# Performance work log

Measured on AMD Instinct MI355X. Metric: run time of the kernel, lower is better.

## Reference

```python
import jax, jax.numpy as jnp
import numpy as np

WIN = 8
NUM_HEADS = 4
DIM = 128


def _relative_position_index(ws):
    coords = np.stack(np.meshgrid(np.arange(ws), np.arange(ws), indexing='ij'))  # (2, ws, ws)
    cf = coords.reshape(2, -1)                      # (2, ws*ws)
    rel = (cf[:, :, None] - cf[:, None, :]).transpose(1, 2, 0).astype(np.int64)  # (N, N, 2)
    rel[..., 0] += ws - 1
    rel[..., 1] += ws - 1
    rel[..., 0] *= 2 * ws - 1
    return rel.sum(-1)                              # (N, N) int64


def setup_inputs() -> dict:
    key = jax.random.key(0)
    ks = jax.random.split(key, 8)
    B_, N, C = 4096, WIN * WIN, DIM
    nW = 4096
    x = jax.random.normal(ks[0], (B_, N, C), dtype=jnp.float32)
    mask = jax.random.normal(ks[1], (nW, N, N), dtype=jnp.float32)
    wq = jax.random.normal(ks[2], (C, C), dtype=jnp.float32) * 0.02
    bq = jnp.zeros((C,), dtype=jnp.float32)
    wkv = jax.random.normal(ks[3], (2 * C, C), dtype=jnp.float32) * 0.02
    bkv = jnp.zeros((2 * C,), dtype=jnp.float32)
    bias_table = jax.random.normal(ks[4], ((2 * WIN - 1) * (2 * WIN - 1), NUM_HEADS), dtype=jnp.float32) * 0.02
    wproj = jax.random.normal(ks[5], (C, C), dtype=jnp.float32) * 0.02
    bproj = jnp.zeros((C,), dtype=jnp.float32)
    rel_index = jnp.asarray(_relative_position_index(WIN))
    return {"x": x, "wq": wq, "bq": bq, "wkv": wkv, "bkv": bkv,
            "bias_table": bias_table, "wproj": wproj, "bproj": bproj,
            "mask": mask, "rel_index": rel_index}


def reference(x, wq, bq, wkv, bkv, bias_table, wproj, bproj, mask, rel_index):
    B_, N, C = x.shape
    H = NUM_HEADS
    d = C // H
    scale = d ** -0.5
    # qkv projection (attn_kv=None path)
    q = (x @ wq.T + bq).reshape(B_, N, H, d).transpose(0, 2, 1, 3)      # (B_, H, N, d)
    kv = (x @ wkv.T + bkv).reshape(B_, N, 2, H, d)
    k = kv[:, :, 0].transpose(0, 2, 1, 3)                               # (B_, H, N, d)
    v = kv[:, :, 1].transpose(0, 2, 1, 3)
    attn = jnp.einsum('bhnd,bhmd->bhnm', q * scale, k)                  # (B_, H, N, N)
    # relative position bias gather: (N*N,) -> (N, N, H) -> (H, N, N)
    rpb = bias_table[rel_index.reshape(-1)].reshape(N, N, H).transpose(2, 0, 1)
    attn = attn + rpb[None]
    # shifted-window mask: attn viewed as (B_//nW, nW, H, N, N) + mask (nW, 1, N, N)
    nW = mask.shape[0]
    attn = (attn.reshape(B_ // nW, nW, H, N, N) + mask[None, :, None]).reshape(B_, H, N, N)
    attn = jax.nn.softmax(attn, axis=-1)
    out = jnp.einsum('bhnm,bhmd->bhnd', attn, v).transpose(0, 2, 1, 3).reshape(B_, N, C)
    return out @ wproj.T + bproj
```

## Files before the change

### kernel.cpp

```cpp
#include <hip/hip_runtime.h>


typedef __bf16 bf16x8 __attribute__((ext_vector_type(8)));
typedef __bf16 bf16x4 __attribute__((ext_vector_type(4)));
typedef float f32x4 __attribute__((ext_vector_type(4)));

#define LOG2E 1.4426950408889634f
#define QSCALE (0.17677669529663687f * 1.4426950408889634f)

__global__ __launch_bounds__(256)
void prep_kernel(const float* __restrict__ wq,
                 const float* __restrict__ wkv,
                 const float* __restrict__ wp,
                 const float* __restrict__ bt,
                 const int* __restrict__ ri,
                 char* __restrict__ ws) {
  int t = blockIdx.x * 256 + (int)threadIdx.x;
  if (t < 8192) {
    int s = t >> 11;
    int c = t & 2047;
    int lane = c & 63, kk = (c >> 6) & 3, ct = c >> 8;
    int li = lane & 15, q4 = lane >> 4;
    int col = ct * 16 + li;
    int ko = kk * 32 + q4 * 8;
    const float* src = (s == 0) ? (wq + col * 128 + ko)
                     : (s == 1) ? (wkv + col * 128 + ko)
                     : (s == 2) ? (wkv + (col + 128) * 128 + ko)
                                : (wp + col * 128 + ko);
    bf16x8 v;
#pragma unroll
    for (int i = 0; i < 8; ++i) v[i] = (__bf16)src[i];
    *(bf16x8*)(ws + s * 32768 + c * 16) = v;
  } else {
    int c = t - 8192;
    int lane = c & 63, tj = (c >> 6) & 3, ti = (c >> 8) & 3, h = (c >> 10) & 3;
    int li = lane & 15, q4 = lane >> 4;
    int qt = tj * 16 + li;
    f32x4 r;
#pragma unroll
    for (int rr = 0; rr < 4; ++rr) {
      int kt = ti * 16 + q4 * 4 + rr;
      r[rr] = LOG2E * bt[ri[qt * 64 + kt] * 4 + h];
    }
    *(f32x4*)(ws + 131072 + c * 16) = r;
  }
}

static __device__ __forceinline__ bf16x8 cvt8nt(const float* __restrict__ p) {
  f32x4 a = __builtin_nontemporal_load((const f32x4*)p);
  f32x4 b = __builtin_nontemporal_load((const f32x4*)p + 1);
  bf16x8 r;
#pragma unroll
  for (int i = 0; i < 4; ++i) { r[i] = (__bf16)a[i]; r[i + 4] = (__bf16)b[i]; }
  return r;
}

static __device__ __forceinline__ int xaddr(int r, int c) {
  return (r << 8) + ((((c >> 3) ^ (r & 7)) << 4)) + ((c & 7) << 1);
}
static __device__ __forceinline__ int qaddr(int r, int c) {
  return (r << 6) + ((((c >> 3) ^ ((r >> 2) & 3)) << 4)) + ((c & 7) << 1);
}
static __device__ __forceinline__ int paddr(int r, int c) {
  return (r << 7) + ((((c >> 3) ^ (r & 7)) << 4)) + ((c & 7) << 1);
}
static __device__ __forceinline__ int vtaddr(int dd, int m) {
  return (dd << 7) + ((((m >> 3) ^ (dd & 7)) << 4)) + ((m & 7) << 1);
}

#define MFMA16(acc, afr, bfr) \
  acc = __builtin_amdgcn_mfma_f32_16x16x32_bf16(afr, bfr, acc, 0, 0, 0)

__global__ __launch_bounds__(256, 3)
void winattn_kernel(const float* __restrict__ xg,
                    const float* __restrict__ bq,
                    const float* __restrict__ bkv,
                    const float* __restrict__ bp,
                    const float* __restrict__ mask,
                    const char* __restrict__ ws,
                    float* __restrict__ out) {
  __shared__ char smem[49152];
  const int b = blockIdx.x;
  const int tid = (int)threadIdx.x;
  const int h = tid >> 6;
  const int lane = tid & 63;
  const int q4 = lane >> 4;
  const int li = lane & 15;
  const int Wb = 16384 + h * 8192;
  const int Qb = Wb, Kb = Wb + 4096, Pb = Wb;
  const int Vb = h * 4096;
  const bf16x8* __restrict__ wqP = (const bf16x8*)(ws);
  const bf16x8* __restrict__ wkP = (const bf16x8*)(ws + 32768);
  const bf16x8* __restrict__ wvP = (const bf16x8*)(ws + 65536);
  const bf16x8* __restrict__ wpP = (const bf16x8*)(ws + 98304);
  const f32x4* __restrict__ rpbP = (const f32x4*)(ws + 131072);

  {
    const float* xw = xg + b * 8192;
#pragma unroll
    for (int rep = 0; rep < 4; ++rep) {
      int chunk = rep * 256 + tid;
      int r = chunk >> 4, cc = chunk & 15;
      bf16x8 v = cvt8nt(xw + r * 128 + cc * 8);
      *(bf16x8*)(smem + xaddr(r, cc * 8)) = v;
    }
  }
  __syncthreads();

  {
    f32x4 aqT[2][4] = {}; f32x4 akT[2][4] = {}; f32x4 av[4][2] = {};
#pragma unroll
    for (int kk = 0; kk < 4; ++kk) {
      bf16x8 a[4];
#pragma unroll
      for (int nt = 0; nt < 4; ++nt)
        a[nt] = *(const bf16x8*)(smem + xaddr(nt * 16 + li, kk * 32 + q4 * 8));
#pragma unroll
      for (int mt = 0; mt < 2; ++mt) {
        int wi = ((h * 2 + mt) * 4 + kk) * 64 + lane;
        bf16x8 wbq = wqP[wi];
        bf16x8 wbk = wkP[wi];
        bf16x8 wbv = wvP[wi];
#pragma unroll
        for (int nt = 0; nt < 4; ++nt) {
          MFMA16(aqT[mt][nt], wbq, a[nt]);
          MFMA16(akT[mt][nt], wbk, a[nt]);
          MFMA16(av[nt][mt], a[nt], wbv);
        }
      }
    }
#pragma unroll
    for (int mt = 0; mt < 2; ++mt) {
      f32x4 bq4 = *(const f32x4*)(bq + h * 32 + mt * 16 + q4 * 4);
      f32x4 bk4 = *(const f32x4*)(bkv + h * 32 + mt * 16 + q4 * 4);
      int f0 = mt * 16 + q4 * 4;
#pragma unroll
      for (int nt = 0; nt < 4; ++nt) {
        bf16x4 qv, kv;
#pragma unroll
        for (int rr = 0; rr < 4; ++rr) {
          qv[rr] = (__bf16)((aqT[mt][nt][rr] + bq4[rr]) * QSCALE);
          kv[rr] = (__bf16)(akT[mt][nt][rr] + bk4[rr]);
        }
        int row = nt * 16 + li;
        *(bf16x4*)(smem + Qb + qaddr(row, f0)) = qv;
        *(bf16x4*)(smem + Kb + qaddr(row, f0)) = kv;
      }
    }
    __syncthreads();
#pragma unroll
    for (int tj = 0; tj < 2; ++tj) {
      int col = h * 32 + tj * 16 + li;
      float bvv = bkv[col + 128];
      int lc = tj * 16 + li;
#pragma unroll
      for (int ti = 0; ti < 4; ++ti) {
        bf16x4 vv;
#pragma unroll
        for (int rr = 0; rr < 4; ++rr) vv[rr] = (__bf16)(av[ti][tj][rr] + bvv);
        *(bf16x4*)(smem + Vb + vtaddr(lc, ti * 16 + q4 * 4)) = vv;
      }
    }
  }
  asm volatile("s_waitcnt lgkmcnt(0)" ::: "memory");

  f32x4 bias[4][4];
  {
    const float* mw = mask + b * 4096;
#pragma unroll
    for (int ti = 0; ti < 4; ++ti)
#pragma unroll
      for (int tj = 0; tj < 4; ++tj) {
        f32x4 rv = rpbP[((h * 4 + ti) * 4 + tj) * 64 + lane];
        f32x4 mv = __builtin_nontemporal_load(
            (const f32x4*)(mw + (tj * 16 + li) * 64 + ti * 16 + q4 * 4));
#pragma unroll
        for (int rr = 0; rr < 4; ++rr) rv[rr] = fmaf(LOG2E, mv[rr], rv[rr]);
        bias[ti][tj] = rv;
      }
  }

  f32x4 S[4][4];
  {
    bf16x8 qf[4], kf[4];
#pragma unroll
    for (int t = 0; t < 4; ++t) {
      qf[t] = *(const bf16x8*)(smem + Qb + qaddr(t * 16 + li, q4 * 8));
      kf[t] = *(const bf16x8*)(smem + Kb + qaddr(t * 16 + li, q4 * 8));
    }
#pragma unroll
    for (int ti = 0; ti < 4; ++ti)
#pragma unroll
      for (int tj = 0; tj < 4; ++tj)
        S[ti][tj] = __builtin_amdgcn_mfma_f32_16x16x32_bf16(
            kf[ti], qf[tj], bias[ti][tj], 0, 0, 0);
  }

#pragma unroll
  for (int tj = 0; tj < 4; ++tj) {
    float mx = S[0][tj][0];
#pragma unroll
    for (int ti = 0; ti < 4; ++ti)
#pragma unroll
      for (int rr = 0; rr < 4; ++rr) mx = fmaxf(mx, S[ti][tj][rr]);
    mx = fmaxf(mx, __shfl_xor(mx, 16));
    mx = fmaxf(mx, __shfl_xor(mx, 32));
    float s = 0.f;
#pragma unroll
    for (int ti = 0; ti < 4; ++ti)
#pragma unroll
      for (int rr = 0; rr < 4; ++rr) {
        float e = __builtin_amdgcn_exp2f(S[ti][tj][rr] - mx);
        S[ti][tj][rr] = e;
        s += e;
      }
    s += __shfl_xor(s, 16);
    s += __shfl_xor(s, 32);
    float rinv = __builtin_amdgcn_rcpf(s);
#pragma unroll
    for (int ti = 0; ti < 4; ++ti)
#pragma unroll
      for (int rr = 0; rr < 4; ++rr) S[ti][tj][rr] *= rinv;
  }

#pragma unroll
  for (int ti = 0; ti < 4; ++ti)
#pragma unroll
    for (int tj = 0; tj < 4; ++tj) {
      bf16x4 pv;
#pragma unroll
      for (int rr = 0; rr < 4; ++rr) pv[rr] = (__bf16)S[ti][tj][rr];
      *(bf16x4*)(smem + Pb + paddr(tj * 16 + li, ti * 16 + q4 * 4)) = pv;
    }
  asm volatile("s_waitcnt lgkmcnt(0)" ::: "memory");

  f32x4 O[4][2] = {};
#pragma unroll
  for (int ks = 0; ks < 2; ++ks) {
    bf16x8 pf[4], vf[2];
#pragma unroll
    for (int ti = 0; ti < 4; ++ti)
      pf[ti] = *(const bf16x8*)(smem + Pb + paddr(ti * 16 + li, ks * 32 + q4 * 8));
#pragma unroll
    for (int tj = 0; tj < 2; ++tj)
      vf[tj] = *(const bf16x8*)(smem + Vb + vtaddr(tj * 16 + li, ks * 32 + q4 * 8));
#pragma unroll
    for (int ti = 0; ti < 4; ++ti)
#pragma unroll
      for (int tj = 0; tj < 2; ++tj)
        MFMA16(O[ti][tj], pf[ti], vf[tj]);
  }

  __syncthreads();
#pragma unroll
  for (int ti = 0; ti < 4; ++ti)
#pragma unroll
    for (int tj = 0; tj < 2; ++tj)
#pragma unroll
      for (int rr = 0; rr < 4; ++rr) {
        int row = ti * 16 + q4 * 4 + rr;
        int col = h * 32 + tj * 16 + li;
        *(__bf16*)(smem + xaddr(row, col)) = (__bf16)O[ti][tj][rr];
      }
  __syncthreads();

  {
    f32x4 acc[2][4] = {};
#pragma unroll
    for (int kk = 0; kk < 4; ++kk) {
      bf16x8 a[4];
#pragma unroll
      for (int nt = 0; nt < 4; ++nt)
        a[nt] = *(const bf16x8*)(smem + xaddr(nt * 16 + li, kk * 32 + q4 * 8));
#pragma unroll
      for (int mt = 0; mt < 2; ++mt) {
        int wi = ((h * 2 + mt) * 4 + kk) * 64 + lane;
        bf16x8 wb = wpP[wi];
#pragma unroll
        for (int nt = 0; nt < 4; ++nt)
          MFMA16(acc[mt][nt], wb, a[nt]);
      }
    }
    float* ow = out + b * 8192;
#pragma unroll
    for (int mt = 0; mt < 2; ++mt) {
      f32x4 bp4 = *(const f32x4*)(bp + h * 32 + mt * 16 + q4 * 4);
#pragma unroll
      for (int nt = 0; nt < 4; ++nt) {
        f32x4 o;
#pragma unroll
        for (int rr = 0; rr < 4; ++rr) o[rr] = acc[mt][nt][rr] + bp4[rr];
        __builtin_nontemporal_store(
            o, (f32x4*)(ow + (nt * 16 + li) * 128 + h * 32 + mt * 16 + q4 * 4));
      }
    }
  }
}

extern "C" void kernel_launch(void* const* d_in, const int* in_sizes, int n_in,
                              void* d_out, int out_size, void* d_ws, size_t ws_size,
                              hipStream_t stream) {
  (void)in_sizes; (void)n_in; (void)ws_size; (void)out_size;
  prep_kernel<<<96, 256, 0, stream>>>(
      (const float*)d_in[1],
      (const float*)d_in[3],
      (const float*)d_in[6],
      (const float*)d_in[5],
      (const int*)d_in[9],
      (char*)d_ws);
  winattn_kernel<<<4096, 256, 0, stream>>>(
      (const float*)d_in[0],
      (const float*)d_in[2],
      (const float*)d_in[4],
      (const float*)d_in[7],
      (const float*)d_in[8],
      (const char*)d_ws,
      (float*)d_out);
}
```

Baseline: 389.3 us.

## Process four windows per block with register-prefetched next-window input

Each block now loops over four windows instead of one. While the current window is computed, the next window's x tile is loaded into registers and written to a separate shared-memory region once the QKV stage is done, so global load latency overlaps compute. Shared memory grows to 64KB, occupancy drops to 2 blocks per CU, and the grid shrinks to 1024 blocks. Nontemporal loads and stores are replaced by ordinary ones. Fewer resident waves and extra register pressure from the prefetch buffer may limit latency hiding.

```diff
diff --git a/kernel.cpp b/kernel.cpp
--- a/kernel.cpp
+++ b/kernel.cpp
@@ -46,15 +46,6 @@
   }
 }
 
-static __device__ __forceinline__ bf16x8 cvt8nt(const float* __restrict__ p) {
-  f32x4 a = __builtin_nontemporal_load((const f32x4*)p);
-  f32x4 b = __builtin_nontemporal_load((const f32x4*)p + 1);
-  bf16x8 r;
-#pragma unroll
-  for (int i = 0; i < 4; ++i) { r[i] = (__bf16)a[i]; r[i + 4] = (__bf16)b[i]; }
-  return r;
-}
-
 static __device__ __forceinline__ int xaddr(int r, int c) {
   return (r << 8) + ((((c >> 3) ^ (r & 7)) << 4)) + ((c & 7) << 1);
 }
@@ -71,7 +62,7 @@
 #define MFMA16(acc, afr, bfr) \
   acc = __builtin_amdgcn_mfma_f32_16x16x32_bf16(afr, bfr, acc, 0, 0, 0)
 
-__global__ __launch_bounds__(256, 3)
+__global__ __launch_bounds__(256, 2)
 void winattn_kernel(const float* __restrict__ xg,
                     const float* __restrict__ bq,
                     const float* __restrict__ bkv,
@@ -79,79 +70,126 @@
                     const float* __restrict__ mask,
                     const char* __restrict__ ws,
                     float* __restrict__ out) {
-  __shared__ char smem[49152];
-  const int b = blockIdx.x;
+  __shared__ char smem[65536];
   const int tid = (int)threadIdx.x;
   const int h = tid >> 6;
   const int lane = tid & 63;
   const int q4 = lane >> 4;
   const int li = lane & 15;
-  const int Wb = 16384 + h * 8192;
-  const int Qb = Wb, Kb = Wb + 4096, Pb = Wb;
-  const int Vb = h * 4096;
+  const int YB = 16384;
+  const int Vb = 16384 + h * 4096;
+  const int Qb = 32768 + h * 8192;
+  const int Kb = Qb + 4096;
+  const int Pb = Qb;
   const bf16x8* __restrict__ wqP = (const bf16x8*)(ws);
   const bf16x8* __restrict__ wkP = (const bf16x8*)(ws + 32768);
   const bf16x8* __restrict__ wvP = (const bf16x8*)(ws + 65536);
   const bf16x8* __restrict__ wpP = (const bf16x8*)(ws + 98304);
   const f32x4* __restrict__ rpbP = (const f32x4*)(ws + 131072);
 
+  const int b0 = blockIdx.x * 4;
+  f32x4 px[8];
+
   {
-    const float* xw = xg + b * 8192;
+    const float* xw = xg + (size_t)b0 * 8192;
 #pragma unroll
     for (int rep = 0; rep < 4; ++rep) {
-      int chunk = rep * 256 + tid;
-      int r = chunk >> 4, cc = chunk & 15;
-      bf16x8 v = cvt8nt(xw + r * 128 + cc * 8);
+      int ch = rep * 256 + tid;
+      int r = ch >> 4, cc = ch & 15;
+      px[2 * rep] = *(const f32x4*)(xw + r * 128 + cc * 8);
+      px[2 * rep + 1] = *(const f32x4*)(xw + r * 128 + cc * 8 + 4);
+    }
+#pragma unroll
+    for (int rep = 0; rep < 4; ++rep) {
+      int ch = rep * 256 + tid;
+      int r = ch >> 4, cc = ch & 15;
+      bf16x8 v;
+#pragma unroll
+      for (int i = 0; i < 4; ++i) {
+        v[i] = (__bf16)px[2 * rep][i];
+        v[i + 4] = (__bf16)px[2 * rep + 1][i];
+      }
       *(bf16x8*)(smem + xaddr(r, cc * 8)) = v;
     }
   }
   __syncthreads();
 
-  {
-    f32x4 aqT[2][4] = {}; f32x4 akT[2][4] = {}; f32x4 av[4][2] = {};
-#pragma unroll
-    for (int kk = 0; kk < 4; ++kk) {
-      bf16x8 a[4];
-#pragma unroll
-      for (int nt = 0; nt < 4; ++nt)
-        a[nt] = *(const bf16x8*)(smem + xaddr(nt * 16 + li, kk * 32 + q4 * 8));
+#pragma unroll 1
+  for (int it = 0; it < 4; ++it) {
+    const int b = b0 + it;
+
+    if (it < 3) {
+      const float* xw = xg + (size_t)(b + 1) * 8192;
+#pragma unroll
+      for (int rep = 0; rep < 4; ++rep) {
+        int ch = rep * 256 + tid;
+        int r = ch >> 4, cc = ch & 15;
+        px[2 * rep] = *(const f32x4*)(xw + r * 128 + cc * 8);
+        px[2 * rep + 1] = *(const f32x4*)(xw + r * 128 + cc * 8 + 4);
+      }
+    }
+
+    f32x4 av[4][2] = {};
+    {
+      f32x4 aqT[2][4] = {}; f32x4 akT[2][4] = {};
+#pragma unroll
+      for (int kk = 0; kk < 4; ++kk) {
+        bf16x8 a[4];
+#pragma unroll
+        for (int nt = 0; nt < 4; ++nt)
+          a[nt] = *(const bf16x8*)(smem + xaddr(nt * 16 + li, kk * 32 + q4 * 8));
+#pragma unroll
+        for (int mt = 0; mt < 2; ++mt) {
+          int wi = ((h * 2 + mt) * 4 + kk) * 64 + lane;
+          bf16x8 wbq = wqP[wi];
+          bf16x8 wbk = wkP[wi];
+          bf16x8 wbv = wvP[wi];
+#pragma unroll
+          for (int nt = 0; nt < 4; ++nt) {
+            MFMA16(aqT[mt][nt], wbq, a[nt]);
+            MFMA16(akT[mt][nt], wbk, a[nt]);
+            MFMA16(av[nt][mt], a[nt], wbv);
+          }
+        }
+      }
 #pragma unroll
       for (int mt = 0; mt < 2; ++mt) {
-        int wi = ((h * 2 + mt) * 4 + kk) * 64 + lane;
-        bf16x8 wbq = wqP[wi];
-        bf16x8 wbk = wkP[wi];
-        bf16x8 wbv = wvP[wi];
+        f32x4 bq4 = *(const f32x4*)(bq + h * 32 + mt * 16 + q4 * 4);
+        f32x4 bk4 = *(const f32x4*)(bkv + h * 32 + mt * 16 + q4 * 4);
+        int f0 = mt * 16 + q4 * 4;
 #pragma unroll
         for (int nt = 0; nt < 4; ++nt) {
-          MFMA16(aqT[mt][nt], wbq, a[nt]);
-          MFMA16(akT[mt][nt], wbk, a[nt]);
-          MFMA16(av[nt][mt], a[nt], wbv);
-        }
-      }
-    }
-#pragma unroll
-    for (int mt = 0; mt < 2; ++mt) {
-      f32x4 bq4 = *(const f32x4*)(bq + h * 32 + mt * 16 + q4 * 4);
-      f32x4 bk4 = *(const f32x4*)(bkv + h * 32 + mt * 16 + q4 * 4);
-      int f0 = mt * 16 + q4 * 4;
-#pragma unroll
-      for (int nt = 0; nt < 4; ++nt) {
-        bf16x4 qv, kv;
-#pragma unroll
-        for (int rr = 0; rr < 4; ++rr) {
-          qv[rr] = (__bf16)((aqT[mt][nt][rr] + bq4[rr]) * QSCALE);
-          kv[rr] = (__bf16)(akT[mt][nt][rr] + bk4[rr]);
-        }
-        int row = nt * 16 + li;
-        *(bf16x4*)(smem + Qb + qaddr(row, f0)) = qv;
-        *(bf16x4*)(smem + Kb + qaddr(row, f0)) = kv;
+          bf16x4 qv, kv;
+#pragma unroll
+          for (int rr = 0; rr < 4; ++rr) {
+            qv[rr] = (__bf16)((aqT[mt][nt][rr] + bq4[rr]) * QSCALE);
+            kv[rr] = (__bf16)(akT[mt][nt][rr] + bk4[rr]);
+          }
+          int row = nt * 16 + li;
+          *(bf16x4*)(smem + Qb + qaddr(row, f0)) = qv;
+          *(bf16x4*)(smem + Kb + qaddr(row, f0)) = kv;
+        }
       }
     }
     __syncthreads();
+
+    if (it < 3) {
+#pragma unroll
+      for (int rep = 0; rep < 4; ++rep) {
+        int ch = rep * 256 + tid;
+        int r = ch >> 4, cc = ch & 15;
+        bf16x8 v;
+#pragma unroll
+        for (int i = 0; i < 4; ++i) {
+          v[i] = (__bf16)px[2 * rep][i];
+          v[i + 4] = (__bf16)px[2 * rep + 1][i];
+        }
+        *(bf16x8*)(smem + xaddr(r, cc * 8)) = v;
+      }
+    }
 #pragma unroll
     for (int tj = 0; tj < 2; ++tj) {
-      int col = h * 32 + tj * 16 + li;
-      float bvv = bkv[col + 128];
+      float bvv = bkv[h * 32 + tj * 16 + li + 128];
       int lc = tj * 16 + li;
 #pragma unroll
       for (int ti = 0; ti < 4; ++ti) {
@@ -161,137 +199,135 @@
         *(bf16x4*)(smem + Vb + vtaddr(lc, ti * 16 + q4 * 4)) = vv;
       }
     }
-  }
-  asm volatile("s_waitcnt lgkmcnt(0)" ::: "memory");
-
-  f32x4 bias[4][4];
-  {
-    const float* mw = mask + b * 4096;
+    asm volatile("s_waitcnt lgkmcnt(0)" ::: "memory");
+
+    f32x4 bias[4][4];
+    {
+      const float* mw = mask + (size_t)b * 4096;
+#pragma unroll
+      for (int ti = 0; ti < 4; ++ti)
+#pragma unroll
+        for (int tj = 0; tj < 4; ++tj) {
+          f32x4 rv = rpbP[((h * 4 + ti) * 4 + tj) * 64 + lane];
+          f32x4 mv = *(const f32x4*)(mw + (tj * 16 + li) * 64 + ti * 16 + q4 * 4);
+#pragma unroll
+          for (int rr = 0; rr < 4; ++rr) rv[rr] = fmaf(LOG2E, mv[rr], rv[rr]);
+          bias[ti][tj] = rv;
+        }
+    }
+
+    f32x4 S[4][4];
+    {
+      bf16x8 qf[4], kf[4];
+#pragma unroll
+      for (int t = 0; t < 4; ++t) {
+        qf[t] = *(const bf16x8*)(smem + Qb + qaddr(t * 16 + li, q4 * 8));
+        kf[t] = *(const bf16x8*)(smem + Kb + qaddr(t * 16 + li, q4 * 8));
+      }
+#pragma unroll
+      for (int ti = 0; ti < 4; ++ti)
+#pragma unroll
+        for (int tj = 0; tj < 4; ++tj)
+          S[ti][tj] = __builtin_amdgcn_mfma_f32_16x16x32_bf16(
+              kf[ti], qf[tj], bias[ti][tj], 0, 0, 0);
+    }
+
+#pragma unroll
+    for (int tj = 0; tj < 4; ++tj) {
+      float mx = S[0][tj][0];
+#pragma unroll
+      for (int ti = 0; ti < 4; ++ti)
+#pragma unroll
+        for (int rr = 0; rr < 4; ++rr) mx = fmaxf(mx, S[ti][tj][rr]);
+      mx = fmaxf(mx, __shfl_xor(mx, 16));
+      mx = fmaxf(mx, __shfl_xor(mx, 32));
+      float s = 0.f;
+#pragma unroll
+      for (int ti = 0; ti < 4; ++ti)
+#pragma unroll
+        for (int rr = 0; rr < 4; ++rr) {
+          float e = __builtin_amdgcn_exp2f(S[ti][tj][rr] - mx);
+          S[ti][tj][rr] = e;
+          s += e;
+        }
+      s += __shfl_xor(s, 16);
+      s += __shfl_xor(s, 32);
+      float rinv = __builtin_amdgcn_rcpf(s);
+#pragma unroll
+      for (int ti = 0; ti < 4; ++ti)
+#pragma unroll
+        for (int rr = 0; rr < 4; ++rr) S[ti][tj][rr] *= rinv;
+    }
+
 #pragma unroll
     for (int ti = 0; ti < 4; ++ti)
 #pragma unroll
       for (int tj = 0; tj < 4; ++tj) {
-        f32x4 rv = rpbP[((h * 4 + ti) * 4 + tj) * 64 + lane];
-        f32x4 mv = __builtin_nontemporal_load(
-            (const f32x4*)(mw + (tj * 16 + li) * 64 + ti * 16 + q4 * 4));
-#pragma unroll
-        for (int rr = 0; rr < 4; ++rr) rv[rr] = fmaf(LOG2E, mv[rr], rv[rr]);
-        bias[ti][tj] = rv;
-      }
-  }
-
-  f32x4 S[4][4];
-  {
-    bf16x8 qf[4], kf[4];
-#pragma unroll
-    for (int t = 0; t < 4; ++t) {
-      qf[t] = *(const bf16x8*)(smem + Qb + qaddr(t * 16 + li, q4 * 8));
-      kf[t] = *(const bf16x8*)(smem + Kb + qaddr(t * 16 + li, q4 * 8));
-    }
+        bf16x4 pv;
+#pragma unroll
+        for (int rr = 0; rr < 4; ++rr) pv[rr] = (__bf16)S[ti][tj][rr];
+        *(bf16x4*)(smem + Pb + paddr(tj * 16 + li, ti * 16 + q4 * 4)) = pv;
+      }
+    asm volatile("s_waitcnt lgkmcnt(0)" ::: "memory");
+
+    f32x4 O[4][2] = {};
+#pragma unroll
+    for (int ks = 0; ks < 2; ++ks) {
+      bf16x8 pf[4], vf[2];
+#pragma unroll
+      for (int ti = 0; ti < 4; ++ti)
+        pf[ti] = *(const bf16x8*)(smem + Pb + paddr(ti * 16 + li, ks * 32 + q4 * 8));
+#pragma unroll
+      for (int tj = 0; tj < 2; ++tj)
+        vf[tj] = *(const bf16x8*)(smem + Vb + vtaddr(tj * 16 + li, ks * 32 + q4 * 8));
+#pragma unroll
+      for (int ti = 0; ti < 4; ++ti)
+#pragma unroll
+        for (int tj = 0; tj < 2; ++tj)
+          MFMA16(O[ti][tj], pf[ti], vf[tj]);
+    }
+
+    __syncthreads();
 #pragma unroll
     for (int ti = 0; ti < 4; ++ti)
 #pragma unroll
-      for (int tj = 0; tj < 4; ++tj)
-        S[ti][tj] = __builtin_amdgcn_mfma_f32_16x16x32_bf16(
-            kf[ti], qf[tj], bias[ti][tj], 0, 0, 0);
-  }
-
-#pragma unroll
-  for (int tj = 0; tj < 4; ++tj) {
-    float mx = S[0][tj][0];
-#pragma unroll
-    for (int ti = 0; ti < 4; ++ti)
-#pragma unroll
-      for (int rr = 0; rr < 4; ++rr) mx = fmaxf(mx, S[ti][tj][rr]);
-    mx = fmaxf(mx, __shfl_xor(mx, 16));
-    mx = fmaxf(mx, __shfl_xor(mx, 32));
-    float s = 0.f;
-#pragma unroll
-    for (int ti = 0; ti < 4; ++ti)
-#pragma unroll
-      for (int rr = 0; rr < 4; ++rr) {
-        float e = __builtin_amdgcn_exp2f(S[ti][tj][rr] - mx);
-        S[ti][tj][rr] = e;
-        s += e;
-      }
-    s += __shfl_xor(s, 16);
-    s += __shfl_xor(s, 32);
-    float rinv = __builtin_amdgcn_rcpf(s);
-#pragma unroll
-    for (int ti = 0; ti < 4; ++ti)
-#pragma unroll
-      for (int rr = 0; rr < 4; ++rr) S[ti][tj][rr] *= rinv;
-  }
-
-#pragma unroll
-  for (int ti = 0; ti < 4; ++ti)
-#pragma unroll
-    for (int tj = 0; tj < 4; ++tj) {
-      bf16x4 pv;
-#pragma unroll
-      for (int rr = 0; rr < 4; ++rr) pv[rr] = (__bf16)S[ti][tj][rr];
-      *(bf16x4*)(smem + Pb + paddr(tj * 16 + li, ti * 16 + q4 * 4)) = pv;
-    }
-  asm volatile("s_waitcnt lgkmcnt(0)" ::: "memory");
-
-  f32x4 O[4][2] = {};
-#pragma unroll
-  for (int ks = 0; ks < 2; ++ks) {
-    bf16x8 pf[4], vf[2];
-#pragma unroll
-    for (int ti = 0; ti < 4; ++ti)
-      pf[ti] = *(const bf16x8*)(smem + Pb + paddr(ti * 16 + li, ks * 32 + q4 * 8));
-#pragma unroll
-    for (int tj = 0; tj < 2; ++tj)
-      vf[tj] = *(const bf16x8*)(smem + Vb + vtaddr(tj * 16 + li, ks * 32 + q4 * 8));
-#pragma unroll
-    for (int ti = 0; ti < 4; ++ti)
-#pragma unroll
       for (int tj = 0; tj < 2; ++tj)
-        MFMA16(O[ti][tj], pf[ti], vf[tj]);
-  }
-
-  __syncthreads();
-#pragma unroll
-  for (int ti = 0; ti < 4; ++ti)
-#pragma unroll
-    for (int tj = 0; tj < 2; ++tj)
-#pragma unroll
-      for (int rr = 0; rr < 4; ++rr) {
-        int row = ti * 16 + q4 * 4 + rr;
-        int col = h * 32 + tj * 16 + li;
-        *(__bf16*)(smem + xaddr(row, col)) = (__bf16)O[ti][tj][rr];
-      }
-  __syncthreads();
-
-  {
-    f32x4 acc[2][4] = {};
-#pragma unroll
-    for (int kk = 0; kk < 4; ++kk) {
-      bf16x8 a[4];
-#pragma unroll
-      for (int nt = 0; nt < 4; ++nt)
-        a[nt] = *(const bf16x8*)(smem + xaddr(nt * 16 + li, kk * 32 + q4 * 8));
+#pragma unroll
+        for (int rr = 0; rr < 4; ++rr) {
+          int row = ti * 16 + q4 * 4 + rr;
+          int col = h * 32 + tj * 16 + li;
+          *(__bf16*)(smem + YB + xaddr(row, col)) = (__bf16)O[ti][tj][rr];
+        }
+    __syncthreads();
+
+    {
+      f32x4 acc[2][4] = {};
+#pragma unroll
+      for (int kk = 0; kk < 4; ++kk) {
+        bf16x8 a[4];
+#pragma unroll
+        for (int nt = 0; nt < 4; ++nt)
+          a[nt] = *(const bf16x8*)(smem + YB + xaddr(nt * 16 + li, kk * 32 + q4 * 8));
+#pragma unroll
+        for (int mt = 0; mt < 2; ++mt) {
+          int wi = ((h * 2 + mt) * 4 + kk) * 64 + lane;
+          bf16x8 wb = wpP[wi];
+#pragma unroll
+          for (int nt = 0; nt < 4; ++nt)
+            MFMA16(acc[mt][nt], wb, a[nt]);
+        }
+      }
+      float* ow = out + (size_t)b * 8192;
 #pragma unroll
       for (int mt = 0; mt < 2; ++mt) {
-        int wi = ((h * 2 + mt) * 4 + kk) * 64 + lane;
-        bf16x8 wb = wpP[wi];
-#pragma unroll
-        for (int nt = 0; nt < 4; ++nt)
-          MFMA16(acc[mt][nt], wb, a[nt]);
-      }
-    }
-    float* ow = out + b * 8192;
-#pragma unroll
-    for (int mt = 0; mt < 2; ++mt) {
-      f32x4 bp4 = *(const f32x4*)(bp + h * 32 + mt * 16 + q4 * 4);
-#pragma unroll
-      for (int nt = 0; nt < 4; ++nt) {
-        f32x4 o;
-#pragma unroll
-        for (int rr = 0; rr < 4; ++rr) o[rr] = acc[mt][nt][rr] + bp4[rr];
-        __builtin_nontemporal_store(
-            o, (f32x4*)(ow + (nt * 16 + li) * 128 + h * 32 + mt * 16 + q4 * 4));
+        f32x4 bp4 = *(const f32x4*)(bp + h * 32 + mt * 16 + q4 * 4);
+#pragma unroll
+        for (int nt = 0; nt < 4; ++nt) {
+          f32x4 o;
+#pragma unroll
+          for (int rr = 0; rr < 4; ++rr) o[rr] = acc[mt][nt][rr] + bp4[rr];
+          *(f32x4*)(ow + (nt * 16 + li) * 128 + h * 32 + mt * 16 + q4 * 4) = o;
+        }
       }
     }
   }
@@ -308,7 +344,7 @@
       (const float*)d_in[5],
       (const int*)d_in[9],
       (char*)d_ws);
-  winattn_kernel<<<4096, 256, 0, stream>>>(
+  winattn_kernel<<<1024, 256, 0, stream>>>(
       (const float*)d_in[0],
       (const float*)d_in[2],
       (const float*)d_in[4],
```

After: 577.1 us. 48.2% more time.

## Give each head private V buffer, drop barrier, transpose PV output, plain loads

Applied to the files above, without the earlier changes.

Moves each head's V tile into its own shared-memory region so the block-wide barrier between Q/K and V writes can be removed. This grows shared memory from 48KB to 64KB and lowers launch bounds from 3 to 2 blocks per CU. The PV matmul is transposed so the output can be written to shared memory as packed bf16x4 rather than scalar bf16 stores. Nontemporal loads and stores are replaced by ordinary ones, and 64-bit offsets are used. The lower occupancy may reduce how well memory latency is hidden.

```diff
diff --git a/kernel.cpp b/kernel.cpp
--- a/kernel.cpp
+++ b/kernel.cpp
@@ -46,9 +46,9 @@
   }
 }
 
-static __device__ __forceinline__ bf16x8 cvt8nt(const float* __restrict__ p) {
-  f32x4 a = __builtin_nontemporal_load((const f32x4*)p);
-  f32x4 b = __builtin_nontemporal_load((const f32x4*)p + 1);
+static __device__ __forceinline__ bf16x8 cvt8(const float* __restrict__ p) {
+  f32x4 a = *(const f32x4*)p;
+  f32x4 b = *((const f32x4*)p + 1);
   bf16x8 r;
 #pragma unroll
   for (int i = 0; i < 4; ++i) { r[i] = (__bf16)a[i]; r[i + 4] = (__bf16)b[i]; }
@@ -71,7 +71,7 @@
 #define MFMA16(acc, afr, bfr) \
   acc = __builtin_amdgcn_mfma_f32_16x16x32_bf16(afr, bfr, acc, 0, 0, 0)
 
-__global__ __launch_bounds__(256, 3)
+__global__ __launch_bounds__(256, 2)
 void winattn_kernel(const float* __restrict__ xg,
                     const float* __restrict__ bq,
                     const float* __restrict__ bkv,
@@ -79,16 +79,15 @@
                     const float* __restrict__ mask,
                     const char* __restrict__ ws,
                     float* __restrict__ out) {
-  __shared__ char smem[49152];
+  __shared__ char smem[65536];
   const int b = blockIdx.x;
   const int tid = (int)threadIdx.x;
   const int h = tid >> 6;
   const int lane = tid & 63;
   const int q4 = lane >> 4;
   const int li = lane & 15;
-  const int Wb = 16384 + h * 8192;
-  const int Qb = Wb, Kb = Wb + 4096, Pb = Wb;
-  const int Vb = h * 4096;
+  const int Wb = 16384 + h * 12288;
+  const int Qb = Wb, Kb = Wb + 4096, Vb = Wb + 8192, Pb = Wb;
   const bf16x8* __restrict__ wqP = (const bf16x8*)(ws);
   const bf16x8* __restrict__ wkP = (const bf16x8*)(ws + 32768);
   const bf16x8* __restrict__ wvP = (const bf16x8*)(ws + 65536);
@@ -96,12 +95,12 @@
   const f32x4* __restrict__ rpbP = (const f32x4*)(ws + 131072);
 
   {
-    const float* xw = xg + b * 8192;
+    const float* xw = xg + (size_t)b * 8192;
 #pragma unroll
     for (int rep = 0; rep < 4; ++rep) {
       int chunk = rep * 256 + tid;
       int r = chunk >> 4, cc = chunk & 15;
-      bf16x8 v = cvt8nt(xw + r * 128 + cc * 8);
+      bf16x8 v = cvt8(xw + r * 128 + cc * 8);
       *(bf16x8*)(smem + xaddr(r, cc * 8)) = v;
     }
   }
@@ -147,11 +146,9 @@
         *(bf16x4*)(smem + Kb + qaddr(row, f0)) = kv;
       }
     }
-    __syncthreads();
 #pragma unroll
     for (int tj = 0; tj < 2; ++tj) {
-      int col = h * 32 + tj * 16 + li;
-      float bvv = bkv[col + 128];
+      float bvv = bkv[h * 32 + tj * 16 + li + 128];
       int lc = tj * 16 + li;
 #pragma unroll
       for (int ti = 0; ti < 4; ++ti) {
@@ -162,23 +159,22 @@
       }
     }
   }
-  asm volatile("s_waitcnt lgkmcnt(0)" ::: "memory");
 
   f32x4 bias[4][4];
   {
-    const float* mw = mask + b * 4096;
+    const float* mw = mask + (size_t)b * 4096;
 #pragma unroll
     for (int ti = 0; ti < 4; ++ti)
 #pragma unroll
       for (int tj = 0; tj < 4; ++tj) {
         f32x4 rv = rpbP[((h * 4 + ti) * 4 + tj) * 64 + lane];
-        f32x4 mv = __builtin_nontemporal_load(
-            (const f32x4*)(mw + (tj * 16 + li) * 64 + ti * 16 + q4 * 4));
+        f32x4 mv = *(const f32x4*)(mw + (tj * 16 + li) * 64 + ti * 16 + q4 * 4);
 #pragma unroll
         for (int rr = 0; rr < 4; ++rr) rv[rr] = fmaf(LOG2E, mv[rr], rv[rr]);
         bias[ti][tj] = rv;
       }
   }
+  asm volatile("s_waitcnt lgkmcnt(0)" ::: "memory");
 
   f32x4 S[4][4];
   {
@@ -234,34 +230,35 @@
     }
   asm volatile("s_waitcnt lgkmcnt(0)" ::: "memory");
 
-  f32x4 O[4][2] = {};
+  f32x4 OT[2][4] = {};
 #pragma unroll
   for (int ks = 0; ks < 2; ++ks) {
     bf16x8 pf[4], vf[2];
 #pragma unroll
-    for (int ti = 0; ti < 4; ++ti)
-      pf[ti] = *(const bf16x8*)(smem + Pb + paddr(ti * 16 + li, ks * 32 + q4 * 8));
-#pragma unroll
-    for (int tj = 0; tj < 2; ++tj)
-      vf[tj] = *(const bf16x8*)(smem + Vb + vtaddr(tj * 16 + li, ks * 32 + q4 * 8));
-#pragma unroll
-    for (int ti = 0; ti < 4; ++ti)
-#pragma unroll
-      for (int tj = 0; tj < 2; ++tj)
-        MFMA16(O[ti][tj], pf[ti], vf[tj]);
+    for (int nt = 0; nt < 4; ++nt)
+      pf[nt] = *(const bf16x8*)(smem + Pb + paddr(nt * 16 + li, ks * 32 + q4 * 8));
+#pragma unroll
+    for (int mt = 0; mt < 2; ++mt)
+      vf[mt] = *(const bf16x8*)(smem + Vb + vtaddr(mt * 16 + li, ks * 32 + q4 * 8));
+#pragma unroll
+    for (int mt = 0; mt < 2; ++mt)
+#pragma unroll
+      for (int nt = 0; nt < 4; ++nt)
+        MFMA16(OT[mt][nt], vf[mt], pf[nt]);
   }
 
   __syncthreads();
 #pragma unroll
-  for (int ti = 0; ti < 4; ++ti)
-#pragma unroll
-    for (int tj = 0; tj < 2; ++tj)
-#pragma unroll
-      for (int rr = 0; rr < 4; ++rr) {
-        int row = ti * 16 + q4 * 4 + rr;
-        int col = h * 32 + tj * 16 + li;
-        *(__bf16*)(smem + xaddr(row, col)) = (__bf16)O[ti][tj][rr];
-      }
+  for (int mt = 0; mt < 2; ++mt) {
+    int f0 = h * 32 + mt * 16 + q4 * 4;
+#pragma unroll
+    for (int nt = 0; nt < 4; ++nt) {
+      bf16x4 yv;
+#pragma unroll
+      for (int rr = 0; rr < 4; ++rr) yv[rr] = (__bf16)OT[mt][nt][rr];
+      *(bf16x4*)(smem + xaddr(nt * 16 + li, f0)) = yv;
+    }
+  }
   __syncthreads();
 
   {
@@ -281,7 +278,7 @@
           MFMA16(acc[mt][nt], wb, a[nt]);
       }
     }
-    float* ow = out + b * 8192;
+    float* ow = out + (size_t)b * 8192;
 #pragma unroll
     for (int mt = 0; mt < 2; ++mt) {
       f32x4 bp4 = *(const f32x4*)(bp + h * 32 + mt * 16 + q4 * 4);
@@ -290,8 +287,7 @@
         f32x4 o;
 #pragma unroll
         for (int rr = 0; rr < 4; ++rr) o[rr] = acc[mt][nt][rr] + bp4[rr];
-        __builtin_nontemporal_store(
-            o, (f32x4*)(ow + (nt * 16 + li) * 128 + h * 32 + mt * 16 + q4 * 4));
+        *(f32x4*)(ow + (nt * 16 + li) * 128 + h * 32 + mt * 16 + q4 * 4) = o;
       }
     }
   }
```

New measurement: 326.7 us. 16.1% less time.
